# Kernel tuning notes

Hardware: AMD Instinct MI355X
Metric: run time of the kernel (lower is better)

The kernel has to match this reference:

```python
import jax, jax.numpy as jnp
import numpy as np

NUM_TOKENS = 8192
DIM = 256
BETA = 0.25
DECAY = 0.99
EPS = 1e-05


def setup_inputs() -> dict:
    key = jax.random.key(0)
    k1, k2 = jax.random.split(key, 2)
    z = jax.random.normal(k1, (16, DIM, 32, 32), dtype=jnp.float32)
    embedding = jax.random.normal(k2, (NUM_TOKENS, DIM), dtype=jnp.float32)
    cluster_size = jnp.zeros((NUM_TOKENS,), dtype=jnp.float32)
    ema_w = embedding  # module init copies embed_init into both embedding and ema_w
    return {"z": z, "embedding": embedding, "cluster_size": cluster_size, "ema_w": ema_w}


def reference(z, embedding, cluster_size, ema_w):
    # z: [B, D, H, W] -> [B, H, W, D]
    zp = jnp.transpose(z, (0, 2, 3, 1))
    zf = zp.reshape(-1, DIM)  # [N, D]
    # squared euclidean distances [N, K] via ||z||^2 + ||e||^2 - 2 z.e
    d = (jnp.sum(zf * zf, axis=1, keepdims=True)
         + jnp.sum(embedding * embedding, axis=1)
         - 2.0 * (zf @ embedding.T))
    idx = jnp.argmin(d, axis=1)  # [N]
    z_q = embedding[idx].reshape(zp.shape)  # [B, H, W, D]

    # training-mode EMA statistics (pure-functional: returned as new states)
    counts = jax.ops.segment_sum(jnp.ones(zf.shape[0], dtype=zf.dtype), idx,
                                 num_segments=NUM_TOKENS)
    embed_sum = jax.ops.segment_sum(zf, idx, num_segments=NUM_TOKENS)  # [K, D]
    cs = cluster_size * DECAY + (1.0 - DECAY) * counts
    new_ema_w = ema_w * DECAY + (1.0 - DECAY) * embed_sum
    # torch evaluates sum AFTER add_(eps): denom = sum(cs + eps) + K*eps
    cs = cs + EPS
    new_cluster_size = cs / (jnp.sum(cs) + NUM_TOKENS * EPS)
    new_embedding = new_ema_w / new_cluster_size[:, None]

    loss = BETA * jnp.mean((jax.lax.stop_gradient(z_q) - zp) ** 2)
    # straight-through estimator
    z_q_st = zp + jax.lax.stop_gradient(z_q - zp)
    out = jnp.transpose(z_q_st, (0, 3, 1, 2))  # back to [B, D, H, W]
    return out, loss, idx, new_cluster_size, new_ema_w, new_embedding
```

## Files before the change

### kernel.cpp

```cpp
#include <hip/hip_runtime.h>

#define N_TOK   16384
#define K_CODES 8192
#define DIMS    256

#define OUT_OFF  0
#define LOSS_OFF 4194304
#define IDX_OFF  4194305
#define NCS_OFF  4210689
#define NEMA_OFF 4218881
#define NEMB_OFF 6316033

#define WS_ZFRAG  0u
#define WS_EFRAG  16777216u
#define WS_ENORM  25165824u
#define WS_AMIN   25198592u
#define WS_IDXI   25722880u
#define WS_CNT    25788416u
#define WS_CS     25821184u
#define WS_OFFS   25853952u
#define WS_WPOS   25886720u
#define WS_TLIST  25919488u
#define WS_DENOM  25985024u

typedef _Float16 f16x8 __attribute__((ext_vector_type(8)));
typedef float    f32x16 __attribute__((ext_vector_type(16)));

union HU { _Float16 h; unsigned short u; };

static __device__ inline void split_f32(float x, unsigned short& hi, unsigned short& lo) {
    HU a; a.h = (_Float16)x;
    float r = (x - (float)a.h) * 2048.0f;
    HU b; b.h = (_Float16)r;
    hi = a.u; lo = b.u;
}

static __device__ inline float join_f16(unsigned short h, unsigned short l) {
    HU a, b; a.u = h; b.u = l;
    return (float)a.h + (float)b.h * 4.8828125e-4f;
}

#define GLD16(gp, lp) __builtin_amdgcn_global_load_lds( \
    (const __attribute__((address_space(1))) unsigned int*)(gp), \
    (__attribute__((address_space(3))) unsigned int*)(lp), 16, 0, 0)

__global__ __launch_bounds__(256) void fused_cvt(
    const float* __restrict__ z, unsigned short* __restrict__ zfrag,
    float* __restrict__ loss_cell, double* __restrict__ denom,
    const float* __restrict__ emb, unsigned short* __restrict__ efrag,
    float* __restrict__ enorm, int* __restrict__ cnt,
    unsigned long long* __restrict__ amin) {
    const int t = threadIdx.x;
    if (blockIdx.x < 1024) {
        __shared__ float T[64][65];
        const int hg = blockIdx.x & 15, dg = (blockIdx.x >> 4) & 3, b = blockIdx.x >> 6;
        if (blockIdx.x == 0 && t == 0) { *loss_cell = 0.f; *denom = 0.0; }
        const int c4 = (t & 15) * 4, r0 = t >> 4;
        const float* zb = z + (((size_t)(b * 256 + dg * 64)) << 10) + hg * 64;
#pragma unroll
        for (int p = 0; p < 4; ++p) {
            const int r = r0 + p * 16;
            const float4 v = *(const float4*)(zb + ((size_t)r << 10) + c4);
            T[r][c4] = v.x; T[r][c4 + 1] = v.y; T[r][c4 + 2] = v.z; T[r][c4 + 3] = v.w;
        }
        __syncthreads();
        const int tr = t & 63, dc = (t >> 6) * 16;
        const int tile = b * 16 + hg;
        const int tg = tile * 2 + (tr >> 5), l31 = tr & 31;
        const int ks = dg * 4 + (dc >> 4);
        unsigned short hb[16], lb[16];
#pragma unroll
        for (int j = 0; j < 16; ++j) split_f32(T[dc + j][tr], hb[j], lb[j]);
#pragma unroll
        for (int lv = 0; lv < 2; ++lv) {
            const unsigned short* src = lv ? lb : hb;
            unsigned short* dst = zfrag + (size_t)((tg * 2 + lv) * 16 + ks) * 512;
            *(uint4*)(dst + l31 * 8)       = ((const uint4*)src)[0];
            *(uint4*)(dst + 256 + l31 * 8) = ((const uint4*)src)[1];
        }
    } else {
        __shared__ double red[256];
        const int g = blockIdx.x - 1024;
        const int lane = t & 63, q = t >> 6;
        const int l31 = lane & 31, lhi = lane >> 5;
        if (g < 32) cnt[g * 256 + t] = 0;
        if (g < 64) amin[g * 256 + t] = 0xFFFFFFFFFFFFFFFFull;
        const float* rowp = emb + (size_t)(g * 32 + l31) * 256 + lhi * 8;
        double s = 0.0;
#pragma unroll
        for (int kk = 0; kk < 4; ++kk) {
            const int ks = q * 4 + kk;
            const float4 a = *(const float4*)(rowp + ks * 16);
            const float4 bq = *(const float4*)(rowp + ks * 16 + 4);
            const float vv[8] = {a.x, a.y, a.z, a.w, bq.x, bq.y, bq.z, bq.w};
            unsigned short hb[8], lb[8];
#pragma unroll
            for (int j = 0; j < 8; ++j) {
                split_f32(vv[j], hb[j], lb[j]);
                s += (double)vv[j] * (double)vv[j];
            }
            *(uint4*)(efrag + (size_t)((g * 2 + 0) * 16 + ks) * 512 + lane * 8) = *(const uint4*)hb;
            *(uint4*)(efrag + (size_t)((g * 2 + 1) * 16 + ks) * 512 + lane * 8) = *(const uint4*)lb;
        }
        red[t] = s;
        __syncthreads();
        if (t < 32) {
            double acc = 0.0;
#pragma unroll
            for (int qq = 0; qq < 4; ++qq) acc += red[qq * 64 + t] + red[qq * 64 + 32 + t];
            enorm[g * 32 + t] = (float)acc;
        }
    }
}

__global__ __launch_bounds__(256, 2) void argmin_mfma(
    const unsigned short* __restrict__ zfrag, const unsigned short* __restrict__ efrag,
    const float* __restrict__ enorm, unsigned long long* __restrict__ amin) {
    __shared__ __align__(16) unsigned short E[2][8192];
    __shared__ float en_s[2][64];

    const int tid = threadIdx.x, lane = tid & 63, wave = tid >> 6;
    const int tile = blockIdx.x & 127, csplit = blockIdx.x >> 7;
    const int token0 = tile * 128, code0 = csplit * 2048;

    f16x8 Zr[2][16];
    {
        const unsigned short* zb = zfrag + (size_t)(tile * 4 + wave) * 16384 + lane * 8;
#pragma unroll
        for (int lv = 0; lv < 2; ++lv)
#pragma unroll
            for (int ks = 0; ks < 16; ++ks)
                Zr[lv][ks] = *(const f16x8*)(zb + (lv * 16 + ks) * 512);
    }

    const int slv = wave >> 1, scg = wave & 1;

    float bv = 3.4e38f; int bi = 0;

#pragma unroll
    for (int ksl = 0; ksl < 4; ++ksl) {
        const unsigned short* sp = efrag +
            (size_t)(((csplit * 64 + scg) * 2 + slv) * 16 + ksl) * 512 + lane * 8;
        GLD16(sp, &E[0][(wave * 4 + ksl) * 512]);
    }
    if (tid < 64) en_s[0][tid] = enorm[code0 + tid];
    __syncthreads();

    for (int ct = 0; ct < 32; ++ct) {
        f32x16 acc_h[2], acc_l[2];
#pragma unroll
        for (int cg = 0; cg < 2; ++cg)
#pragma unroll
            for (int qq = 0; qq < 16; ++qq) { acc_h[cg][qq] = 0.f; acc_l[cg][qq] = 0.f; }

#pragma unroll
        for (int kc = 0; kc < 4; ++kc) {
            const int p = (ct * 4 + kc) & 1;
            if (!(ct == 31 && kc == 3)) {
                const int nch = ct * 4 + kc + 1;
                const int nct = nch >> 2, nkc = nch & 3;
                const int g = csplit * 64 + nct * 2 + scg;
#pragma unroll
                for (int ksl = 0; ksl < 4; ++ksl) {
                    const unsigned short* sp = efrag +
                        (size_t)((g * 2 + slv) * 16 + nkc * 4 + ksl) * 512 + lane * 8;
                    GLD16(sp, &E[p ^ 1][(wave * 4 + ksl) * 512]);
                }
            }
            if (kc == 0 && ct < 31 && tid < 64)
                en_s[(ct + 1) & 1][tid] = enorm[code0 + (ct + 1) * 64 + tid];

#pragma unroll
            for (int ksl = 0; ksl < 4; ++ksl) {
                const int ks = kc * 4 + ksl;
                f16x8 ae[2][2];
#pragma unroll
                for (int lv = 0; lv < 2; ++lv)
#pragma unroll
                    for (int cg = 0; cg < 2; ++cg)
                        ae[lv][cg] = *(const f16x8*)&E[p][((lv * 2 + cg) * 4 + ksl) * 512 + lane * 8];
#pragma unroll
                for (int cg = 0; cg < 2; ++cg)
                    acc_h[cg] = __builtin_amdgcn_mfma_f32_32x32x16_f16(ae[0][cg], Zr[0][ks], acc_h[cg], 0, 0, 0);
#pragma unroll
                for (int cg = 0; cg < 2; ++cg)
                    acc_l[cg] = __builtin_amdgcn_mfma_f32_32x32x16_f16(ae[0][cg], Zr[1][ks], acc_l[cg], 0, 0, 0);
#pragma unroll
                for (int cg = 0; cg < 2; ++cg)
                    acc_l[cg] = __builtin_amdgcn_mfma_f32_32x32x16_f16(ae[1][cg], Zr[0][ks], acc_l[cg], 0, 0, 0);
            }
            if (kc == 3) {
                const int rbase = 4 * (lane >> 5);
#pragma unroll
                for (int cg = 0; cg < 2; ++cg)
#pragma unroll
                    for (int r = 0; r < 16; ++r) {
                        const int cl = cg * 32 + (r & 3) + 8 * (r >> 2) + rbase;
                        const float s = en_s[ct & 1][cl] -
                            2.0f * (acc_h[cg][r] + acc_l[cg][r] * 4.8828125e-4f);
                        const int code = code0 + ct * 64 + cl;
                        if (s < bv) { bv = s; bi = code; }
                    }
            }
            __syncthreads();
        }
    }
    {
        const float ov = __shfl_xor(bv, 32);
        const int   oi = __shfl_xor(bi, 32);
        if (ov < bv || (ov == bv && oi < bi)) { bv = ov; bi = oi; }
    }
    if (lane < 32) {
        const int n = token0 + wave * 32 + lane;
        unsigned int u = __float_as_uint(bv);
        u = (u & 0x80000000u) ? ~u : (u | 0x80000000u);
        const unsigned long long pk = ((unsigned long long)u << 32) | (unsigned int)bi;
        atomicMin(&amin[n], pk);
    }
}

__global__ __launch_bounds__(256) void idx_cnt_kernel(
    const unsigned long long* __restrict__ amin,
    int* __restrict__ idx_i, float* __restrict__ idx_f, int* __restrict__ cnt) {
    const int n = blockIdx.x * 256 + threadIdx.x;
    const int bi = (int)(unsigned int)(amin[n] & 0xFFFFFFFFull);
    idx_i[n] = bi;
    idx_f[n] = (float)bi;
    atomicAdd(&cnt[bi], 1);
}

__global__ __launch_bounds__(256) void scan_kernel(const int* __restrict__ cnt,
                                                   int* __restrict__ offs,
                                                   int* __restrict__ wpos) {
    __shared__ int part[256];
    const int tid = threadIdx.x;
    const int base = tid * 32;
    int loc[32];
    int s = 0;
#pragma unroll
    for (int j = 0; j < 32; ++j) { loc[j] = cnt[base + j]; s += loc[j]; }
    part[tid] = s;
    __syncthreads();
    for (int off = 1; off < 256; off <<= 1) {
        int v = 0;
        if (tid >= off) v = part[tid - off];
        __syncthreads();
        if (tid >= off) part[tid] += v;
        __syncthreads();
    }
    int run = (tid > 0) ? part[tid - 1] : 0;
#pragma unroll
    for (int j = 0; j < 32; ++j) {
        offs[base + j] = run;
        wpos[base + j] = run;
        run += loc[j];
    }
}

__global__ __launch_bounds__(256) void scatter_cs(
    const int* __restrict__ idx_i, int* __restrict__ wpos, int* __restrict__ tlist,
    const float* __restrict__ cluster_size, const int* __restrict__ cnt,
    float* __restrict__ cs, double* __restrict__ denom) {
    __shared__ double red[256];
    const int t = threadIdx.x, b = blockIdx.x;
    if (b < 64) {
        const int n = b * 256 + t;
        const int k = idx_i[n];
        tlist[atomicAdd(&wpos[k], 1)] = n;
    } else {
        const int k = (b - 64) * 256 + t;
        const float v = cluster_size[k] * 0.99f + 0.01f * (float)cnt[k] + 1e-5f;
        cs[k] = v;
        red[t] = (double)v;
        __syncthreads();
        for (int s2 = 128; s2; s2 >>= 1) {
            if (t < s2) red[t] += red[t + s2];
            __syncthreads();
        }
        if (t == 0) atomicAdd(denom, red[0]);
    }
}

__global__ __launch_bounds__(256) void nema_gather(
    const unsigned short* __restrict__ zfrag,
    const int* __restrict__ offs, const int* __restrict__ cnt, const int* __restrict__ tlist,
    const float* __restrict__ ema_w, const float* __restrict__ cs,
    const double* __restrict__ denom, float* __restrict__ ncs_out,
    float* __restrict__ nema_out, float* __restrict__ nemb_out,
    const float* __restrict__ z, const float* __restrict__ emb,
    const int* __restrict__ idx_i, float* __restrict__ out, float* __restrict__ loss_cell) {
    __shared__ float redf[256];
    const int t = threadIdx.x;
    if (blockIdx.x < 2048) {
        const int lane = t & 63, wave = t >> 6;
        const int k = blockIdx.x * 4 + wave;
        const int l31 = lane & 31, sel = lane >> 5;
        const int beg = offs[k], c = cnt[k];
        float acc[8] = {0.f, 0.f, 0.f, 0.f, 0.f, 0.f, 0.f, 0.f};
        const size_t lidx = (size_t)((l31 >> 1) + sel * 16) * 512 + (l31 & 1) * 256;
        int i = 0;
        for (; i + 1 < c; i += 2) {
            const int tokA = tlist[beg + i], tokB = tlist[beg + i + 1];
            const uint4 vA = *(const uint4*)(zfrag + (size_t)(tokA >> 5) * 16384 + lidx + (tokA & 31) * 8);
            const uint4 vB = *(const uint4*)(zfrag + (size_t)(tokB >> 5) * 16384 + lidx + (tokB & 31) * 8);
            uint4 oA, oB;
            oA.x = __shfl_xor((int)vA.x, 32); oA.y = __shfl_xor((int)vA.y, 32);
            oA.z = __shfl_xor((int)vA.z, 32); oA.w = __shfl_xor((int)vA.w, 32);
            oB.x = __shfl_xor((int)vB.x, 32); oB.y = __shfl_xor((int)vB.y, 32);
            oB.z = __shfl_xor((int)vB.z, 32); oB.w = __shfl_xor((int)vB.w, 32);
            if (lane < 32) {
                const unsigned short* hA = (const unsigned short*)&vA;
                const unsigned short* lA = (const unsigned short*)&oA;
                const unsigned short* hB = (const unsigned short*)&vB;
                const unsigned short* lB = (const unsigned short*)&oB;
#pragma unroll
                for (int j = 0; j < 8; ++j)
                    acc[j] += join_f16(hA[j], lA[j]) + join_f16(hB[j], lB[j]);
            }
        }
        if (i < c) {
            const int tok = tlist[beg + i];
            const uint4 v = *(const uint4*)(zfrag + (size_t)(tok >> 5) * 16384 + lidx + (tok & 31) * 8);
            uint4 o;
            o.x = __shfl_xor((int)v.x, 32); o.y = __shfl_xor((int)v.y, 32);
            o.z = __shfl_xor((int)v.z, 32); o.w = __shfl_xor((int)v.w, 32);
            if (lane < 32) {
                const unsigned short* hp = (const unsigned short*)&v;
                const unsigned short* lp = (const unsigned short*)&o;
#pragma unroll
                for (int j = 0; j < 8; ++j) acc[j] += join_f16(hp[j], lp[j]);
            }
        }
        const float dn = (float)(*denom) + (float)K_CODES * 1e-5f;
        const float ncs = cs[k] / dn;
        if (lane == 0) ncs_out[k] = ncs;
        if (lane < 32) {
            const size_t off = ((size_t)k << 8) + l31 * 8;
#pragma unroll
            for (int j = 0; j < 8; ++j) {
                const float ne = ema_w[off + j] * 0.99f + 0.01f * acc[j];
                nema_out[off + j] = ne;
                nemb_out[off + j] = ne / ncs;
            }
        }
    } else {
        const int gb = blockIdx.x - 2048;
        const int n0 = (gb >> 2) * 64;
        const int dg = (gb & 3) * 64;
        const int b = n0 >> 10, hw0 = n0 & 1023;
        const int lane = t & 63, w = t >> 6;
        const int n = n0 + lane;
        const int k = idx_i[n];
        const float* zb = z + ((size_t)b << 18) + hw0 + lane;
        float* ob = out + ((size_t)b << 18) + hw0 + lane;
        float ls = 0.f;
#pragma unroll 4
        for (int d = dg + w; d < dg + 64; d += 4) {
            const float zv = zb[(size_t)d << 10];
            const float ev = emb[((size_t)k << 8) + d];
            ob[(size_t)d << 10] = ev;
            const float df = ev - zv;
            ls += df * df;
        }
        redf[t] = ls;
        __syncthreads();
        for (int s2 = 128; s2; s2 >>= 1) {
            if (t < s2) redf[t] += redf[t + s2];
            __syncthreads();
        }
        if (t == 0) atomicAdd(loss_cell, redf[0] * (0.25f / 4194304.0f));
    }
}

extern "C" void kernel_launch(void* const* d_in, const int* in_sizes, int n_in,
                              void* d_out, int out_size, void* d_ws, size_t ws_size,
                              hipStream_t stream) {
    const float* z            = (const float*)d_in[0];
    const float* emb          = (const float*)d_in[1];
    const float* cluster_size = (const float*)d_in[2];
    const float* ema_w        = (const float*)d_in[3];
    float* out = (float*)d_out;
    char*  wsb = (char*)d_ws;

    unsigned short* zfrag = (unsigned short*)(wsb + WS_ZFRAG);
    unsigned short* efrag = (unsigned short*)(wsb + WS_EFRAG);
    float*  enorm  = (float*)(wsb + WS_ENORM);
    unsigned long long* amin = (unsigned long long*)(wsb + WS_AMIN);
    int*    idx_i  = (int*)(wsb + WS_IDXI);
    int*    cnt    = (int*)(wsb + WS_CNT);
    float*  cs     = (float*)(wsb + WS_CS);
    int*    offs   = (int*)(wsb + WS_OFFS);
    int*    wpos   = (int*)(wsb + WS_WPOS);
    int*    tlist  = (int*)(wsb + WS_TLIST);
    double* denom  = (double*)(wsb + WS_DENOM);

    fused_cvt<<<1280, 256, 0, stream>>>(z, zfrag, out + LOSS_OFF, denom,
                                        emb, efrag, enorm, cnt, amin);
    argmin_mfma<<<512, 256, 0, stream>>>(zfrag, efrag, enorm, amin);
    idx_cnt_kernel<<<N_TOK / 256, 256, 0, stream>>>(amin, idx_i, out + IDX_OFF, cnt);
    scan_kernel<<<1, 256, 0, stream>>>(cnt, offs, wpos);
    scatter_cs<<<96, 256, 0, stream>>>(idx_i, wpos, tlist, cluster_size, cnt, cs, denom);
    nema_gather<<<3072, 256, 0, stream>>>(zfrag, offs, cnt, tlist, ema_w, cs, denom,
                                          out + NCS_OFF, out + NEMA_OFF, out + NEMB_OFF,
                                          z, emb, idx_i, out + OUT_OFF, out + LOSS_OFF);
}
```

Baseline: 375.5 us.

## Stream low-half codebook fragments directly to registers, halving LDS staging

The argmin kernel now stages only the high-precision half of the codebook fragments through shared memory. The low-order correction fragments are loaded straight from global memory into registers, double-buffered two k-steps ahead. This halves LDS footprint and traffic. Block indexing is also changed so the four code splits of one token tile run on adjacent blocks, which may improve L2 reuse of the Z tile. The cost is more in-flight global loads and extra register pressure, plus exposed latency if the register prefetch is not far enough ahead.

```diff
diff --git a/kernel.cpp b/kernel.cpp
--- a/kernel.cpp
+++ b/kernel.cpp
@@ -116,11 +116,11 @@
 __global__ __launch_bounds__(256, 2) void argmin_mfma(
     const unsigned short* __restrict__ zfrag, const unsigned short* __restrict__ efrag,
     const float* __restrict__ enorm, unsigned long long* __restrict__ amin) {
-    __shared__ __align__(16) unsigned short E[2][8192];
+    __shared__ __align__(16) unsigned short E[2][4096];
     __shared__ float en_s[2][64];
 
     const int tid = threadIdx.x, lane = tid & 63, wave = tid >> 6;
-    const int tile = blockIdx.x & 127, csplit = blockIdx.x >> 7;
+    const int csplit = blockIdx.x & 3, tile = blockIdx.x >> 2;
     const int token0 = tile * 128, code0 = csplit * 2048;
 
     f16x8 Zr[2][16];
@@ -133,17 +133,33 @@
                 Zr[lv][ks] = *(const f16x8*)(zb + (lv * 16 + ks) * 512);
     }
 
-    const int slv = wave >> 1, scg = wave & 1;
+    const int scg = wave & 1, kb = (wave >> 1) * 2;
+    auto stage_hi = [&](int ch, int buf) {
+        const int nct = ch >> 2, nkc = ch & 3;
+        const int g = csplit * 64 + nct * 2 + scg;
+#pragma unroll
+        for (int k2 = 0; k2 < 2; ++k2) {
+            const int ksl = kb + k2;
+            const unsigned short* sp = efrag +
+                (size_t)((g * 2 + 0) * 16 + nkc * 4 + ksl) * 512 + lane * 8;
+            GLD16(sp, &E[buf][(scg * 4 + ksl) * 512]);
+        }
+    };
+
+    const unsigned short* lobase = efrag + ((size_t)csplit << 20) + 8192 + lane * 8;
+    f16x8 lo[2][2];
+    auto issue_lo = [&](int ct_, int k_, f16x8* buf) {
+#pragma unroll
+        for (int cg = 0; cg < 2; ++cg)
+            buf[cg] = *(const f16x8*)(lobase + ((size_t)ct_ << 15) + (cg << 14) + (k_ << 9));
+    };
 
     float bv = 3.4e38f; int bi = 0;
 
-#pragma unroll
-    for (int ksl = 0; ksl < 4; ++ksl) {
-        const unsigned short* sp = efrag +
-            (size_t)(((csplit * 64 + scg) * 2 + slv) * 16 + ksl) * 512 + lane * 8;
-        GLD16(sp, &E[0][(wave * 4 + ksl) * 512]);
-    }
+    stage_hi(0, 0);
     if (tid < 64) en_s[0][tid] = enorm[code0 + tid];
+    issue_lo(0, 0, lo[0]);
+    issue_lo(0, 1, lo[1]);
     __syncthreads();
 
     for (int ct = 0; ct < 32; ++ct) {
@@ -156,39 +172,31 @@
 #pragma unroll
         for (int kc = 0; kc < 4; ++kc) {
             const int p = (ct * 4 + kc) & 1;
-            if (!(ct == 31 && kc == 3)) {
-                const int nch = ct * 4 + kc + 1;
-                const int nct = nch >> 2, nkc = nch & 3;
-                const int g = csplit * 64 + nct * 2 + scg;
-#pragma unroll
-                for (int ksl = 0; ksl < 4; ++ksl) {
-                    const unsigned short* sp = efrag +
-                        (size_t)((g * 2 + slv) * 16 + nkc * 4 + ksl) * 512 + lane * 8;
-                    GLD16(sp, &E[p ^ 1][(wave * 4 + ksl) * 512]);
-                }
-            }
+            if (!(ct == 31 && kc == 3)) stage_hi(ct * 4 + kc + 1, p ^ 1);
             if (kc == 0 && ct < 31 && tid < 64)
                 en_s[(ct + 1) & 1][tid] = enorm[code0 + (ct + 1) * 64 + tid];
 
 #pragma unroll
             for (int ksl = 0; ksl < 4; ++ksl) {
-                const int ks = kc * 4 + ksl;
-                f16x8 ae[2][2];
-#pragma unroll
-                for (int lv = 0; lv < 2; ++lv)
-#pragma unroll
-                    for (int cg = 0; cg < 2; ++cg)
-                        ae[lv][cg] = *(const f16x8*)&E[p][((lv * 2 + cg) * 4 + ksl) * 512 + lane * 8];
+                const int k = kc * 4 + ksl;
+                f16x8 ae0[2];
 #pragma unroll
                 for (int cg = 0; cg < 2; ++cg)
-                    acc_h[cg] = __builtin_amdgcn_mfma_f32_32x32x16_f16(ae[0][cg], Zr[0][ks], acc_h[cg], 0, 0, 0);
+                    ae0[cg] = *(const f16x8*)&E[p][(cg * 4 + ksl) * 512 + lane * 8];
 #pragma unroll
                 for (int cg = 0; cg < 2; ++cg)
-                    acc_l[cg] = __builtin_amdgcn_mfma_f32_32x32x16_f16(ae[0][cg], Zr[1][ks], acc_l[cg], 0, 0, 0);
+                    acc_h[cg] = __builtin_amdgcn_mfma_f32_32x32x16_f16(ae0[cg], Zr[0][k], acc_h[cg], 0, 0, 0);
 #pragma unroll
                 for (int cg = 0; cg < 2; ++cg)
-                    acc_l[cg] = __builtin_amdgcn_mfma_f32_32x32x16_f16(ae[1][cg], Zr[0][ks], acc_l[cg], 0, 0, 0);
-            }
+                    acc_l[cg] = __builtin_amdgcn_mfma_f32_32x32x16_f16(ae0[cg], Zr[1][k], acc_l[cg], 0, 0, 0);
+#pragma unroll
+                for (int cg = 0; cg < 2; ++cg)
+                    acc_l[cg] = __builtin_amdgcn_mfma_f32_32x32x16_f16(lo[k & 1][cg], Zr[0][k], acc_l[cg], 0, 0, 0);
+                const int kn = k + 2;
+                if (kn < 16)       issue_lo(ct, kn, lo[k & 1]);
+                else if (ct < 31)  issue_lo(ct + 1, kn - 16, lo[k & 1]);
+            }
+
             if (kc == 3) {
                 const int rbase = 4 * (lane >> 5);
 #pragma unroll
```

After: 397.7 us. 1.06x slower.

## Merge idx/count, scan and scatter kernels into one kernel with grid barriers

Applied to the files above, without the earlier changes.

Replaces three small launches (index extraction and counting, single-block scan, scatter plus cluster-size reduction) with one 64-block kernel. Two software grid barriers built from atomic counters and spin-waits separate the phases. This removes two kernel launches and their inter-kernel gaps. It relies on all 64 blocks being co-resident, and spin-waiting on a global counter adds contention and a hang risk if that ever fails.

```diff
diff --git a/kernel.cpp b/kernel.cpp
--- a/kernel.cpp
+++ b/kernel.cpp
@@ -49,7 +49,7 @@
     float* __restrict__ loss_cell, double* __restrict__ denom,
     const float* __restrict__ emb, unsigned short* __restrict__ efrag,
     float* __restrict__ enorm, int* __restrict__ cnt,
-    unsigned long long* __restrict__ amin) {
+    unsigned long long* __restrict__ amin, int* __restrict__ bar) {
     const int t = threadIdx.x;
     if (blockIdx.x < 1024) {
         __shared__ float T[64][65];
@@ -85,6 +85,7 @@
         const int l31 = lane & 31, lhi = lane >> 5;
         if (g < 32) cnt[g * 256 + t] = 0;
         if (g < 64) amin[g * 256 + t] = 0xFFFFFFFFFFFFFFFFull;
+        if (g == 0 && t < 2) bar[t] = 0;
         const float* rowp = emb + (size_t)(g * 32 + l31) * 256 + lhi * 8;
         double s = 0.0;
 #pragma unroll
@@ -219,58 +220,58 @@
     }
 }
 
-__global__ __launch_bounds__(256) void idx_cnt_kernel(
+__global__ __launch_bounds__(256) void post_kernel(
     const unsigned long long* __restrict__ amin,
-    int* __restrict__ idx_i, float* __restrict__ idx_f, int* __restrict__ cnt) {
-    const int n = blockIdx.x * 256 + threadIdx.x;
-    const int bi = (int)(unsigned int)(amin[n] & 0xFFFFFFFFull);
-    idx_i[n] = bi;
-    idx_f[n] = (float)bi;
-    atomicAdd(&cnt[bi], 1);
-}
-
-__global__ __launch_bounds__(256) void scan_kernel(const int* __restrict__ cnt,
-                                                   int* __restrict__ offs,
-                                                   int* __restrict__ wpos) {
-    __shared__ int part[256];
-    const int tid = threadIdx.x;
-    const int base = tid * 32;
-    int loc[32];
-    int s = 0;
-#pragma unroll
-    for (int j = 0; j < 32; ++j) { loc[j] = cnt[base + j]; s += loc[j]; }
-    part[tid] = s;
+    int* __restrict__ idx_i, float* __restrict__ idx_f,
+    int* __restrict__ cnt, int* __restrict__ offs, int* __restrict__ wpos,
+    int* __restrict__ tlist, const float* __restrict__ cluster_size,
+    float* __restrict__ cs, double* __restrict__ denom, int* __restrict__ bar) {
+    const int t = threadIdx.x, b = blockIdx.x;
+    const int n = b * 256 + t;
+    const int k = (int)(unsigned int)(amin[n] & 0xFFFFFFFFull);
+    idx_i[n] = k;
+    idx_f[n] = (float)k;
+    atomicAdd(&cnt[k], 1);
+
+    __threadfence();
     __syncthreads();
-    for (int off = 1; off < 256; off <<= 1) {
-        int v = 0;
-        if (tid >= off) v = part[tid - off];
+    if (t == 0) {
+        atomicAdd(&bar[0], 1);
+        while (__hip_atomic_load(&bar[0], __ATOMIC_RELAXED, __HIP_MEMORY_SCOPE_AGENT) < 64) {}
+    }
+    __syncthreads();
+
+    if (b == 0) {
+        __shared__ int part[256];
+        const int base = t * 32;
+        int loc[32]; int s = 0;
+#pragma unroll
+        for (int j = 0; j < 32; ++j) {
+            loc[j] = __hip_atomic_load(&cnt[base + j], __ATOMIC_RELAXED, __HIP_MEMORY_SCOPE_AGENT);
+            s += loc[j];
+        }
+        part[t] = s;
         __syncthreads();
-        if (tid >= off) part[tid] += v;
-        __syncthreads();
-    }
-    int run = (tid > 0) ? part[tid - 1] : 0;
-#pragma unroll
-    for (int j = 0; j < 32; ++j) {
-        offs[base + j] = run;
-        wpos[base + j] = run;
-        run += loc[j];
-    }
-}
-
-__global__ __launch_bounds__(256) void scatter_cs(
-    const int* __restrict__ idx_i, int* __restrict__ wpos, int* __restrict__ tlist,
-    const float* __restrict__ cluster_size, const int* __restrict__ cnt,
-    float* __restrict__ cs, double* __restrict__ denom) {
-    __shared__ double red[256];
-    const int t = threadIdx.x, b = blockIdx.x;
-    if (b < 64) {
-        const int n = b * 256 + t;
-        const int k = idx_i[n];
-        tlist[atomicAdd(&wpos[k], 1)] = n;
-    } else {
-        const int k = (b - 64) * 256 + t;
-        const float v = cluster_size[k] * 0.99f + 0.01f * (float)cnt[k] + 1e-5f;
-        cs[k] = v;
+        for (int off = 1; off < 256; off <<= 1) {
+            int v = 0;
+            if (t >= off) v = part[t - off];
+            __syncthreads();
+            if (t >= off) part[t] += v;
+            __syncthreads();
+        }
+        int run = (t > 0) ? part[t - 1] : 0;
+#pragma unroll
+        for (int j = 0; j < 32; ++j) {
+            offs[base + j] = run;
+            wpos[base + j] = run;
+            run += loc[j];
+        }
+    } else if (b <= 32) {
+        __shared__ double red[256];
+        const int k2 = (b - 1) * 256 + t;
+        const int c = __hip_atomic_load(&cnt[k2], __ATOMIC_RELAXED, __HIP_MEMORY_SCOPE_AGENT);
+        const float v = cluster_size[k2] * 0.99f + 0.01f * (float)c + 1e-5f;
+        cs[k2] = v;
         red[t] = (double)v;
         __syncthreads();
         for (int s2 = 128; s2; s2 >>= 1) {
@@ -279,6 +280,16 @@
         }
         if (t == 0) atomicAdd(denom, red[0]);
     }
+
+    __threadfence();
+    __syncthreads();
+    if (t == 0) {
+        atomicAdd(&bar[1], 1);
+        while (__hip_atomic_load(&bar[1], __ATOMIC_RELAXED, __HIP_MEMORY_SCOPE_AGENT) < 64) {}
+    }
+    __syncthreads();
+
+    tlist[atomicAdd(&wpos[k], 1)] = n;
 }
 
 __global__ __launch_bounds__(256) void nema_gather(
@@ -386,6 +397,7 @@
     unsigned short* efrag = (unsigned short*)(wsb + WS_EFRAG);
     float*  enorm  = (float*)(wsb + WS_ENORM);
     unsigned long long* amin = (unsigned long long*)(wsb + WS_AMIN);
+    int*    bar    = (int*)(wsb + WS_AMIN + 131072);
     int*    idx_i  = (int*)(wsb + WS_IDXI);
     int*    cnt    = (int*)(wsb + WS_CNT);
     float*  cs     = (float*)(wsb + WS_CS);
@@ -395,11 +407,10 @@
     double* denom  = (double*)(wsb + WS_DENOM);
 
     fused_cvt<<<1280, 256, 0, stream>>>(z, zfrag, out + LOSS_OFF, denom,
-                                        emb, efrag, enorm, cnt, amin);
+                                        emb, efrag, enorm, cnt, amin, bar);
     argmin_mfma<<<512, 256, 0, stream>>>(zfrag, efrag, enorm, amin);
-    idx_cnt_kernel<<<N_TOK / 256, 256, 0, stream>>>(amin, idx_i, out + IDX_OFF, cnt);
-    scan_kernel<<<1, 256, 0, stream>>>(cnt, offs, wpos);
-    scatter_cs<<<96, 256, 0, stream>>>(idx_i, wpos, tlist, cluster_size, cnt, cs, denom);
+    post_kernel<<<64, 256, 0, stream>>>(amin, idx_i, out + IDX_OFF, cnt, offs, wpos,
+                                        tlist, cluster_size, cs, denom, bar);
     nema_gather<<<3072, 256, 0, stream>>>(zfrag, offs, cnt, tlist, ema_w, cs, denom,
                                           out + NCS_OFF, out + NEMA_OFF, out + NEMB_OFF,
                                           z, emb, idx_i, out + OUT_OFF, out + LOSS_OFF);
```

Result: slower. 406.7 us (+8.3%).
